# Kernel tuning notes

Hardware: AMD Instinct MI355X
Metric: run time of the kernel (lower is better)

Reference implementation:

```python
import jax, jax.numpy as jnp
import numpy as np

L = 4000      # num identities
C = 8         # num cameras; center bank is label-major: center j -> (label j//C, cam j%C)
T = 0.07      # temperature
HARD_NEG_K = 50
LAMDA = 0.5


def setup_inputs() -> dict:
    key = jax.random.key(0)
    k1, k2, k3, k4 = jax.random.split(key, 4)
    n, d = 256, 2048
    feats = jax.random.normal(k1, (n, d), dtype=jnp.float32)
    centers = jax.random.normal(k2, (L * C, d), dtype=jnp.float32)
    centers = centers / jnp.linalg.norm(centers, axis=1, keepdims=True)  # bank is kept unit-norm
    labels = jax.random.randint(k3, (n,), 0, L, dtype=jnp.int64)
    camids = jax.random.randint(k4, (n,), 0, C, dtype=jnp.int64)
    return {"feats": feats, "centers": centers, "labels": labels, "camids": camids, "epoch": 5}


def _cap_losses(feats, centers, labels, camids):
    n = feats.shape[0]
    M = centers.shape[0]
    feats = feats / jnp.linalg.norm(feats, axis=1, keepdims=True)  # F.normalize(p=2, dim=1)
    center_labels = jnp.arange(M) // C
    center_cams = jnp.arange(M) % C

    sims = jnp.einsum('nd,md->nm', feats, centers) / T  # [n, M] scaled similarities
    own_idx = labels * C + camids                        # cam_label_index[(label, cam)]
    own = sims[jnp.arange(n), own_idx]                   # numerator logits
    exp_sims = jnp.exp(sims)                             # unit vectors => sims <= 1/T ~ 14.3, safe

    # ---- intra-camera loss: denominator over centers sharing the sample's camid ----
    cam_mask = (center_cams[None, :] == camids[:, None])
    denom_intra = jnp.sum(exp_sims * cam_mask, axis=1)
    loss_i = own - jnp.log(denom_intra)                  # log(frac_up/frac_down)
    # mean per camid, then sum over camids present in the batch, negated
    ones = jnp.ones((n,), dtype=feats.dtype)
    cam_sums = jax.ops.segment_sum(loss_i, camids, num_segments=C)
    cam_cnts = jax.ops.segment_sum(ones, camids, num_segments=C)
    loss_intra = -jnp.sum(jnp.where(cam_cnts > 0, cam_sums / jnp.maximum(cam_cnts, 1.0), 0.0))

    # ---- inter loss: same-label centers + first-K hard negatives (in bank order) ----
    lbl_mask = (center_labels[None, :] == labels[:, None])
    other = ~lbl_mask
    # torch concatenates other-label centers in label order and takes the FIRST 50 (a slice,
    # not top-k); label-major bank order makes that = first 50 other-label centers by index.
    rank = jnp.cumsum(other.astype(jnp.int32), axis=1)
    hard_mask = other & (rank <= HARD_NEG_K)
    denom_inter = jnp.sum(exp_sims * lbl_mask, axis=1) + jnp.sum(exp_sims * hard_mask, axis=1)
    loss_j = own - jnp.log(denom_inter)
    lbl_sums = jax.ops.segment_sum(loss_j, labels, num_segments=L)
    lbl_cnts = jax.ops.segment_sum(ones, labels, num_segments=L)
    loss_inter = -jnp.sum(jnp.where(lbl_cnts > 0, lbl_sums / jnp.maximum(lbl_cnts, 1.0), 0.0))

    return loss_intra, loss_inter


def reference(feats, centers, labels, camids, epoch):
    loss_intra, loss_inter = _cap_losses(feats, centers, labels, camids)
    if epoch < 5:  # epoch is a static python int
        return loss_intra
    return jnp.stack([loss_intra, LAMDA * loss_inter])
```

## Files before the change

kernel.cpp:

```cpp
#include <hip/hip_runtime.h>

typedef __attribute__((ext_vector_type(8))) __bf16 bf16x8;
typedef __attribute__((ext_vector_type(4))) __bf16 bf16x4;
typedef __attribute__((ext_vector_type(4))) float f32x4;

#define N_SAMP 256
#define DIM    2048
#define NCENT  32000
#define INV_T  14.285714285714285714f
#define NWG    250

__global__ __launch_bounds__(256) void norm_kernel(const float* __restrict__ feats,
                                                   __bf16* __restrict__ fnorm,
                                                   float* __restrict__ d_acc) {
    int row = blockIdx.x;
    int tid = threadIdx.x;
    if (row < 16) d_acc[row * 256 + tid] = 0.f;
    const float* src = feats + (size_t)row * DIM;
    float4 v0 = reinterpret_cast<const float4*>(src)[2 * tid];
    float4 v1 = reinterpret_cast<const float4*>(src)[2 * tid + 1];
    float ss = v0.x * v0.x + v0.y * v0.y + v0.z * v0.z + v0.w * v0.w
             + v1.x * v1.x + v1.y * v1.y + v1.z * v1.z + v1.w * v1.w;
    #pragma unroll
    for (int off = 1; off < 64; off <<= 1) ss += __shfl_xor(ss, off, 64);
    __shared__ float wsum[4];
    if ((tid & 63) == 0) wsum[tid >> 6] = ss;
    __syncthreads();
    float inv = 1.0f / sqrtf(wsum[0] + wsum[1] + wsum[2] + wsum[3]);
    bf16x8 o;
    o[0] = (__bf16)(v0.x * inv); o[1] = (__bf16)(v0.y * inv);
    o[2] = (__bf16)(v0.z * inv); o[3] = (__bf16)(v0.w * inv);
    o[4] = (__bf16)(v1.x * inv); o[5] = (__bf16)(v1.y * inv);
    o[6] = (__bf16)(v1.z * inv); o[7] = (__bf16)(v1.w * inv);
    *reinterpret_cast<bf16x8*>(fnorm + (size_t)row * DIM + tid * 8) = o;
}

__global__ __launch_bounds__(512, 2) void sims_kernel(
    const __bf16* __restrict__ fnorm, const float* __restrict__ centers,
    const int* __restrict__ labels, const int* __restrict__ camids,
    float* __restrict__ d_acc, float* __restrict__ d_own)
{
    __shared__ __align__(16) char sA[2][16384];
    __shared__ __align__(16) char sB[2][8192];

    const int tid  = threadIdx.x;
    const int wave = tid >> 6;
    const int lane = tid & 63;
    const int l15  = lane & 15;
    const int lhi  = lane >> 4;

    const int nb    = blockIdx.x;
    const int cbase = nb * 128;

    const int wr = (wave >> 1) * 64;
    const int wc = (wave & 1) * 64;

    f32x4 acc[4][4] = {};

    const float4* bsrc = reinterpret_cast<const float4*>(centers);
    const uint4*  asrc = reinterpret_cast<const uint4*>(fnorm);

    auto issue = [&](int step, float4& b0, float4& b1, uint4& a0, uint4& a1) {
        int rb0 = tid >> 3, p = tid & 7;
        b0 = bsrc[(size_t)(cbase + rb0) * 512 + step * 8 + p];
        int rb1 = 64 + rb0;
        b1 = bsrc[(size_t)(cbase + rb1) * 512 + step * 8 + p];
        int ra0 = tid >> 2, pa = tid & 3;
        a0 = asrc[(size_t)ra0 * 256 + step * 4 + pa];
        int ra1 = 128 + ra0;
        a1 = asrc[(size_t)ra1 * 256 + step * 4 + pa];
    };
    auto wrbuf = [&](int b, const float4& b0, const float4& b1,
                     const uint4& a0, const uint4& a1) {
        #pragma unroll
        for (int j = 0; j < 2; ++j) {
            const float4& v = j ? b1 : b0;
            int row = j * 64 + (tid >> 3), pos = tid & 7;
            int adr = (row * 64 + pos * 8) ^ ((row & 7) << 4);
            bf16x4 o;
            o[0] = (__bf16)v.x; o[1] = (__bf16)v.y;
            o[2] = (__bf16)v.z; o[3] = (__bf16)v.w;
            *reinterpret_cast<uint2*>(&sB[b][adr]) = __builtin_bit_cast(uint2, o);
        }
        #pragma unroll
        for (int j = 0; j < 2; ++j) {
            const uint4& v = j ? a1 : a0;
            int row = j * 128 + (tid >> 2), pos = tid & 3;
            int adr = (row * 64 + pos * 16) ^ ((row & 7) << 4);
            *reinterpret_cast<uint4*>(&sA[b][adr]) = v;
        }
    };
    auto compute = [&](int b) {
        bf16x8 af[4], bf[4];
        #pragma unroll
        for (int mi = 0; mi < 4; ++mi) {
            int row = wr + mi * 16 + l15;
            int adr = (row * 64 + lhi * 16) ^ ((row & 7) << 4);
            af[mi] = *reinterpret_cast<const bf16x8*>(&sA[b][adr]);
        }
        #pragma unroll
        for (int ni = 0; ni < 4; ++ni) {
            int row = wc + ni * 16 + l15;
            int adr = (row * 64 + lhi * 16) ^ ((row & 7) << 4);
            bf[ni] = *reinterpret_cast<const bf16x8*>(&sB[b][adr]);
        }
        #pragma unroll
        for (int mi = 0; mi < 4; ++mi)
            #pragma unroll
            for (int ni = 0; ni < 4; ++ni)
                acc[mi][ni] = __builtin_amdgcn_mfma_f32_16x16x32_bf16(
                    af[mi], bf[ni], acc[mi][ni], 0, 0, 0);
    };
    #define BAR() do { asm volatile("s_waitcnt lgkmcnt(0)" ::: "memory"); \
                       __builtin_amdgcn_s_barrier(); } while (0)

    float4 b0A, b1A, b0B, b1B;
    uint4  a0A, a1A, a0B, a1B;

    issue(0, b0A, b1A, a0A, a1A);
    issue(1, b0B, b1B, a0B, a1B);
    wrbuf(0, b0A, b1A, a0A, a1A);
    BAR();
    for (int t = 0; t < 64; t += 2) {
        if (t + 2 < 64) issue(t + 2, b0A, b1A, a0A, a1A);
        compute(0);
        wrbuf(1, b0B, b1B, a0B, a1B);
        BAR();
        if (t + 3 < 64) issue(t + 3, b0B, b1B, a0B, a1B);
        compute(1);
        if (t + 2 < 64) {
            wrbuf(0, b0A, b1A, a0A, a1A);
            BAR();
        }
    }

    float* slot = d_acc + (nb & 7) * 512;
    #pragma unroll
    for (int mi = 0; mi < 4; ++mi) {
        #pragma unroll
        for (int r = 0; r < 4; ++r) {
            int i   = wr + mi * 16 + lhi * 4 + r;
            int lab = labels[i], cam = camids[i];
            int oidx = lab * 8 + cam;
            float pi = 0.f, pj = 0.f;
            #pragma unroll
            for (int ni = 0; ni < 4; ++ni) {
                int c = cbase + wc + ni * 16 + l15;
                float s = acc[mi][ni][r] * INV_T;
                float e = __expf(s);
                if ((l15 & 7) == cam) pi += e;
                bool ol = ((c >> 3) == lab);
                bool hard = (!ol) && (c < ((c < lab * 8) ? 50 : 58));
                if (ol || hard) pj += e;
                if (c == oidx) d_own[i] = s;
            }
            #pragma unroll
            for (int off = 1; off < 16; off <<= 1) {
                pi += __shfl_xor(pi, off, 64);
                pj += __shfl_xor(pj, off, 64);
            }
            if (l15 == 0) {
                atomicAdd(&slot[i], pi);
                atomicAdd(&slot[N_SAMP + i], pj);
            }
        }
    }
}

__global__ __launch_bounds__(256) void finalize_kernel(
    const float* __restrict__ d_acc, const float* __restrict__ d_own,
    const int* __restrict__ labels, const int* __restrict__ camids,
    float* __restrict__ out, int out_size)
{
    __shared__ int s_lab[N_SAMP], s_cam[N_SAMP];
    __shared__ float wsum[8];
    int tid = threadIdx.x;
    s_lab[tid] = labels[tid];
    s_cam[tid] = camids[tid];
    __syncthreads();
    int myl = s_lab[tid], myc = s_cam[tid];
    int nl = 0, nc = 0;
    for (int j = 0; j < N_SAMP; ++j) {
        nl += (s_lab[j] == myl);
        nc += (s_cam[j] == myc);
    }
    float di = 0.f, dj = 0.f;
    #pragma unroll
    for (int s = 0; s < 8; ++s) {
        di += d_acc[s * 512 + tid];
        dj += d_acc[s * 512 + 256 + tid];
    }
    float own = d_own[tid];
    float li = own - logf(di);
    float lj = own - logf(dj);
    float a = li / (float)nc;
    float b = lj / (float)nl;
    #pragma unroll
    for (int off = 1; off < 64; off <<= 1) {
        a += __shfl_xor(a, off, 64);
        b += __shfl_xor(b, off, 64);
    }
    if ((tid & 63) == 0) { wsum[tid >> 6] = a; wsum[4 + (tid >> 6)] = b; }
    __syncthreads();
    if (tid == 0) {
        float sa = wsum[0] + wsum[1] + wsum[2] + wsum[3];
        float sb = wsum[4] + wsum[5] + wsum[6] + wsum[7];
        out[0] = -sa;
        if (out_size > 1) out[1] = -0.5f * sb;
    }
}

extern "C" void kernel_launch(void* const* d_in, const int* in_sizes, int n_in,
                              void* d_out, int out_size, void* d_ws, size_t ws_size,
                              hipStream_t stream) {
    const float* feats   = (const float*)d_in[0];
    const float* centers = (const float*)d_in[1];
    const int*   labels  = (const int*)d_in[2];
    const int*   camids  = (const int*)d_in[3];
    float* out = (float*)d_out;

    __bf16* fnorm = (__bf16*)d_ws;
    float* d_acc  = (float*)((char*)d_ws + (size_t)N_SAMP * DIM * sizeof(__bf16));
    float* d_own  = d_acc + 8 * 2 * N_SAMP;

    norm_kernel<<<N_SAMP, 256, 0, stream>>>(feats, fnorm, d_acc);
    sims_kernel<<<NWG, 512, 0, stream>>>(fnorm, centers, labels, camids, d_acc, d_own);
    finalize_kernel<<<1, 256, 0, stream>>>(d_acc, d_own, labels, camids, out, out_size);
}
```

Measured before the change: 86.05 us.

## Pre-swizzle A tiles, load via global_load_lds, triple-buffer B, fuse finalize

The norm kernel now writes normalized features in a pre-swizzled tile layout, so the GEMM kernel can stream A directly into LDS with global_load_lds instead of staging through registers. B (centers) becomes triple-buffered with one 16-byte store per thread, and uses vmcnt-based waits, setprio around the MFMAs and a fully unrolled loop. The separate finalize launch is replaced by a last-block ticket reduction inside the sims kernel, which removes one kernel launch at the cost of an atomic ticket and threadfences. The fused tail reuses sB shared memory for the finalize scratch.

Measured after the change: 130.7 us. 1.52x slower.

```diff
diff --git a/kernel.cpp b/kernel.cpp
--- a/kernel.cpp
+++ b/kernel.cpp
@@ -1,7 +1,6 @@
 #include <hip/hip_runtime.h>
 
 typedef __attribute__((ext_vector_type(8))) __bf16 bf16x8;
-typedef __attribute__((ext_vector_type(4))) __bf16 bf16x4;
 typedef __attribute__((ext_vector_type(4))) float f32x4;
 
 #define N_SAMP 256
@@ -9,13 +8,17 @@
 #define NCENT  32000
 #define INV_T  14.285714285714285714f
 #define NWG    250
+#define NTILE  64
+
 
 __global__ __launch_bounds__(256) void norm_kernel(const float* __restrict__ feats,
-                                                   __bf16* __restrict__ fnorm,
-                                                   float* __restrict__ d_acc) {
+                                                   char* __restrict__ fnorm_sw,
+                                                   float* __restrict__ d_acc,
+                                                   int* __restrict__ ticket) {
     int row = blockIdx.x;
     int tid = threadIdx.x;
     if (row < 16) d_acc[row * 256 + tid] = 0.f;
+    if (row == 16 && tid == 0) *ticket = 0;
     const float* src = feats + (size_t)row * DIM;
     float4 v0 = reinterpret_cast<const float4*>(src)[2 * tid];
     float4 v1 = reinterpret_cast<const float4*>(src)[2 * tid + 1];
@@ -32,16 +35,20 @@
     o[2] = (__bf16)(v0.z * inv); o[3] = (__bf16)(v0.w * inv);
     o[4] = (__bf16)(v1.x * inv); o[5] = (__bf16)(v1.y * inv);
     o[6] = (__bf16)(v1.z * inv); o[7] = (__bf16)(v1.w * inv);
-    *reinterpret_cast<bf16x8*>(fnorm + (size_t)row * DIM + tid * 8) = o;
+    int tile = tid >> 2, c8 = tid & 3;
+    int pair = row >> 1;
+    int slot = (((row & 1) << 2) | c8) ^ (pair & 7);
+    *reinterpret_cast<bf16x8*>(fnorm_sw + (size_t)tile * 16384 + pair * 128 + slot * 16) = o;
 }
 
 __global__ __launch_bounds__(512, 2) void sims_kernel(
-    const __bf16* __restrict__ fnorm, const float* __restrict__ centers,
+    const char* __restrict__ fnorm_sw, const float* __restrict__ centers,
     const int* __restrict__ labels, const int* __restrict__ camids,
-    float* __restrict__ d_acc, float* __restrict__ d_own)
+    float* __restrict__ d_acc, float* __restrict__ d_own,
+    int* __restrict__ ticket, float* __restrict__ out, int out_size)
 {
     __shared__ __align__(16) char sA[2][16384];
-    __shared__ __align__(16) char sB[2][8192];
+    __shared__ __align__(16) char sB[3][8192];
 
     const int tid  = threadIdx.x;
     const int wave = tid >> 6;
@@ -58,83 +65,84 @@
     f32x4 acc[4][4] = {};
 
     const float4* bsrc = reinterpret_cast<const float4*>(centers);
-    const uint4*  asrc = reinterpret_cast<const uint4*>(fnorm);
-
-    auto issue = [&](int step, float4& b0, float4& b1, uint4& a0, uint4& a1) {
-        int rb0 = tid >> 3, p = tid & 7;
-        b0 = bsrc[(size_t)(cbase + rb0) * 512 + step * 8 + p];
-        int rb1 = 64 + rb0;
-        b1 = bsrc[(size_t)(cbase + rb1) * 512 + step * 8 + p];
-        int ra0 = tid >> 2, pa = tid & 3;
-        a0 = asrc[(size_t)ra0 * 256 + step * 4 + pa];
-        int ra1 = 128 + ra0;
-        a1 = asrc[(size_t)ra1 * 256 + step * 4 + pa];
-    };
-    auto wrbuf = [&](int b, const float4& b0, const float4& b1,
-                     const uint4& a0, const uint4& a1) {
-        #pragma unroll
-        for (int j = 0; j < 2; ++j) {
-            const float4& v = j ? b1 : b0;
-            int row = j * 64 + (tid >> 3), pos = tid & 7;
-            int adr = (row * 64 + pos * 8) ^ ((row & 7) << 4);
-            bf16x4 o;
-            o[0] = (__bf16)v.x; o[1] = (__bf16)v.y;
-            o[2] = (__bf16)v.z; o[3] = (__bf16)v.w;
-            *reinterpret_cast<uint2*>(&sB[b][adr]) = __builtin_bit_cast(uint2, o);
-        }
-        #pragma unroll
-        for (int j = 0; j < 2; ++j) {
-            const uint4& v = j ? a1 : a0;
-            int row = j * 128 + (tid >> 2), pos = tid & 3;
-            int adr = (row * 64 + pos * 16) ^ ((row & 7) << 4);
-            *reinterpret_cast<uint4*>(&sA[b][adr]) = v;
-        }
-    };
-    auto compute = [&](int b) {
+
+    const int bP = tid >> 3, bs = tid & 7;
+    const int bu = bs ^ (bP & 7);
+    const int brow = 2 * bP + (bu >> 2);
+    const int bc8  = bu & 3;
+    const size_t bbase = (size_t)(cbase + brow) * 512 + bc8 * 2;
+
+    auto issueB = [&](int T, float4& f0, float4& f1) {
+        f0 = bsrc[bbase + T * 8];
+        f1 = bsrc[bbase + T * 8 + 1];
+    };
+    auto wrbufB = [&](int buf, const float4& f0, const float4& f1) {
+        bf16x8 o;
+        o[0] = (__bf16)f0.x; o[1] = (__bf16)f0.y; o[2] = (__bf16)f0.z; o[3] = (__bf16)f0.w;
+        o[4] = (__bf16)f1.x; o[5] = (__bf16)f1.y; o[6] = (__bf16)f1.z; o[7] = (__bf16)f1.w;
+        *reinterpret_cast<bf16x8*>(&sB[buf][tid * 16]) = o;
+    };
+    auto aLds = [&](int T, int buf) {
+        const char* src = fnorm_sw + (size_t)T * 16384 + (wave * 2) * 1024 + lane * 16;
+        __builtin_amdgcn_global_load_lds((const unsigned int*)src,
+                                         (unsigned int*)&sA[buf][(wave * 2) * 1024], 16, 0, 0);
+        __builtin_amdgcn_global_load_lds((const unsigned int*)(src + 1024),
+                                         (unsigned int*)&sA[buf][(wave * 2 + 1) * 1024], 16, 0, 0);
+    };
+    auto compute = [&](int bufA, int bufB) {
         bf16x8 af[4], bf[4];
         #pragma unroll
         for (int mi = 0; mi < 4; ++mi) {
-            int row = wr + mi * 16 + l15;
-            int adr = (row * 64 + lhi * 16) ^ ((row & 7) << 4);
-            af[mi] = *reinterpret_cast<const bf16x8*>(&sA[b][adr]);
+            int row = wr + mi * 16 + l15, pair = row >> 1;
+            int slot = (((row & 1) << 2) | lhi) ^ (pair & 7);
+            af[mi] = *reinterpret_cast<const bf16x8*>(&sA[bufA][pair * 128 + slot * 16]);
         }
         #pragma unroll
         for (int ni = 0; ni < 4; ++ni) {
-            int row = wc + ni * 16 + l15;
-            int adr = (row * 64 + lhi * 16) ^ ((row & 7) << 4);
-            bf[ni] = *reinterpret_cast<const bf16x8*>(&sB[b][adr]);
-        }
+            int row = wc + ni * 16 + l15, pair = row >> 1;
+            int slot = (((row & 1) << 2) | lhi) ^ (pair & 7);
+            bf[ni] = *reinterpret_cast<const bf16x8*>(&sB[bufB][pair * 128 + slot * 16]);
+        }
+        __builtin_amdgcn_s_setprio(1);
         #pragma unroll
         for (int mi = 0; mi < 4; ++mi)
             #pragma unroll
             for (int ni = 0; ni < 4; ++ni)
                 acc[mi][ni] = __builtin_amdgcn_mfma_f32_16x16x32_bf16(
                     af[mi], bf[ni], acc[mi][ni], 0, 0, 0);
-    };
-    #define BAR() do { asm volatile("s_waitcnt lgkmcnt(0)" ::: "memory"); \
-                       __builtin_amdgcn_s_barrier(); } while (0)
-
-    float4 b0A, b1A, b0B, b1B;
-    uint4  a0A, a1A, a0B, a1B;
-
-    issue(0, b0A, b1A, a0A, a1A);
-    issue(1, b0B, b1B, a0B, a1B);
-    wrbuf(0, b0A, b1A, a0A, a1A);
-    BAR();
-    for (int t = 0; t < 64; t += 2) {
-        if (t + 2 < 64) issue(t + 2, b0A, b1A, a0A, a1A);
-        compute(0);
-        wrbuf(1, b0B, b1B, a0B, a1B);
-        BAR();
-        if (t + 3 < 64) issue(t + 3, b0B, b1B, a0B, a1B);
-        compute(1);
-        if (t + 2 < 64) {
-            wrbuf(0, b0A, b1A, a0A, a1A);
-            BAR();
+        __builtin_amdgcn_s_setprio(0);
+    };
+
+    float4 b0S0, b1S0, b0S1, b1S1;
+
+    issueB(0, b0S0, b1S0);
+    issueB(1, b0S1, b1S1);
+    aLds(0, 0);
+    wrbufB(0, b0S0, b1S0);
+    asm volatile("s_waitcnt vmcnt(0)" ::: "memory");
+    asm volatile("s_waitcnt lgkmcnt(0)" ::: "memory");
+    __builtin_amdgcn_s_barrier();
+
+    #pragma unroll
+    for (int t = 0; t < NTILE; ++t) {
+        const int cur = t & 1;
+        if (t + 1 < NTILE) aLds(t + 1, cur ^ 1);
+        if (t + 2 < NTILE) {
+            if (((t + 2) & 1) == 0) issueB(t + 2, b0S0, b1S0);
+            else                    issueB(t + 2, b0S1, b1S1);
+        }
+        compute(cur, t % 3);
+        if (t + 1 < NTILE) {
+            if (((t + 1) & 1) == 0) wrbufB((t + 1) % 3, b0S0, b1S0);
+            else                    wrbufB((t + 1) % 3, b0S1, b1S1);
+            if (t + 2 < NTILE) asm volatile("s_waitcnt vmcnt(2)" ::: "memory");
+            else               asm volatile("s_waitcnt vmcnt(0)" ::: "memory");
+            asm volatile("s_waitcnt lgkmcnt(0)" ::: "memory");
+            __builtin_amdgcn_s_barrier();
         }
     }
 
-    float* slot = d_acc + (nb & 7) * 512;
+    float* slot_acc = d_acc + (nb & 7) * 512;
     #pragma unroll
     for (int mi = 0; mi < 4; ++mi) {
         #pragma unroll
@@ -160,53 +168,57 @@
                 pj += __shfl_xor(pj, off, 64);
             }
             if (l15 == 0) {
-                atomicAdd(&slot[i], pi);
-                atomicAdd(&slot[N_SAMP + i], pj);
+                atomicAdd(&slot_acc[i], pi);
+                atomicAdd(&slot_acc[N_SAMP + i], pj);
             }
         }
     }
-}
-
-__global__ __launch_bounds__(256) void finalize_kernel(
-    const float* __restrict__ d_acc, const float* __restrict__ d_own,
-    const int* __restrict__ labels, const int* __restrict__ camids,
-    float* __restrict__ out, int out_size)
-{
-    __shared__ int s_lab[N_SAMP], s_cam[N_SAMP];
-    __shared__ float wsum[8];
-    int tid = threadIdx.x;
-    s_lab[tid] = labels[tid];
-    s_cam[tid] = camids[tid];
+
+    __threadfence();
     __syncthreads();
-    int myl = s_lab[tid], myc = s_cam[tid];
-    int nl = 0, nc = 0;
-    for (int j = 0; j < N_SAMP; ++j) {
-        nl += (s_lab[j] == myl);
-        nc += (s_cam[j] == myc);
-    }
-    float di = 0.f, dj = 0.f;
-    #pragma unroll
-    for (int s = 0; s < 8; ++s) {
-        di += d_acc[s * 512 + tid];
-        dj += d_acc[s * 512 + 256 + tid];
-    }
-    float own = d_own[tid];
-    float li = own - logf(di);
-    float lj = own - logf(dj);
-    float a = li / (float)nc;
-    float b = lj / (float)nl;
-    #pragma unroll
-    for (int off = 1; off < 64; off <<= 1) {
-        a += __shfl_xor(a, off, 64);
-        b += __shfl_xor(b, off, 64);
-    }
-    if ((tid & 63) == 0) { wsum[tid >> 6] = a; wsum[4 + (tid >> 6)] = b; }
+    __shared__ int s_last;
+    if (tid == 0) s_last = (atomicAdd(ticket, 1) == NWG - 1) ? 1 : 0;
     __syncthreads();
-    if (tid == 0) {
-        float sa = wsum[0] + wsum[1] + wsum[2] + wsum[3];
-        float sb = wsum[4] + wsum[5] + wsum[6] + wsum[7];
-        out[0] = -sa;
-        if (out_size > 1) out[1] = -0.5f * sb;
+    if (s_last) {
+        __threadfence();
+        int* s_lab = (int*)&sB[0][0];
+        int* s_cam = s_lab + 256;
+        float* wsum = (float*)(s_cam + 256);
+        if (tid < 256) { s_lab[tid] = labels[tid]; s_cam[tid] = camids[tid]; }
+        __syncthreads();
+        float a = 0.f, b = 0.f;
+        if (tid < 256) {
+            int myl = s_lab[tid], myc = s_cam[tid];
+            int nl = 0, nc = 0;
+            for (int j = 0; j < 256; ++j) {
+                nl += (s_lab[j] == myl);
+                nc += (s_cam[j] == myc);
+            }
+            float di = 0.f, dj = 0.f;
+            #pragma unroll
+            for (int s = 0; s < 8; ++s) {
+                di += d_acc[s * 512 + tid];
+                dj += d_acc[s * 512 + 256 + tid];
+            }
+            float own = d_own[tid];
+            a = (own - logf(di)) / (float)nc;
+            b = (own - logf(dj)) / (float)nl;
+        }
+        #pragma unroll
+        for (int off = 1; off < 64; off <<= 1) {
+            a += __shfl_xor(a, off, 64);
+            b += __shfl_xor(b, off, 64);
+        }
+        if ((tid & 63) == 0) { wsum[tid >> 6] = a; wsum[8 + (tid >> 6)] = b; }
+        __syncthreads();
+        if (tid == 0) {
+            float sa = wsum[0] + wsum[1] + wsum[2] + wsum[3]
+                     + wsum[4] + wsum[5] + wsum[6] + wsum[7];
+            float sb = wsum[8] + wsum[9] + wsum[10] + wsum[11]
+                     + wsum[12] + wsum[13] + wsum[14] + wsum[15];
+            out[0] = -sa;
+            if (out_size > 1) out[1] = -0.5f * sb;
+        }
     }
 }
 
@@ -219,11 +231,12 @@
     const int*   camids  = (const int*)d_in[3];
     float* out = (float*)d_out;
 
-    __bf16* fnorm = (__bf16*)d_ws;
-    float* d_acc  = (float*)((char*)d_ws + (size_t)N_SAMP * DIM * sizeof(__bf16));
-    float* d_own  = d_acc + 8 * 2 * N_SAMP;
-
-    norm_kernel<<<N_SAMP, 256, 0, stream>>>(feats, fnorm, d_acc);
-    sims_kernel<<<NWG, 512, 0, stream>>>(fnorm, centers, labels, camids, d_acc, d_own);
-    finalize_kernel<<<1, 256, 0, stream>>>(d_acc, d_own, labels, camids, out, out_size);
+    char*  fnorm_sw = (char*)d_ws;
+    float* d_acc    = (float*)((char*)d_ws + (size_t)1048576);
+    float* d_own    = d_acc + 8 * 2 * N_SAMP;
+    int*   ticket   = (int*)(d_own + N_SAMP);
+
+    norm_kernel<<<N_SAMP, 256, 0, stream>>>(feats, fnorm_sw, d_acc, ticket);
+    sims_kernel<<<NWG, 512, 0, stream>>>(fnorm_sw, centers, labels, camids,
+                                         d_acc, d_own, ticket, out, out_size);
 }
```

## Pre-pack normalized features in MFMA fragment order and load A directly to registers

Applied to the files above, without the earlier changes.

The norm kernel now writes the bf16 normalized features in a layout that matches the MFMA A-fragment order, so each wave loads its A operands straight from global memory (L2-resident) into registers without staging through LDS. The sA shared buffer goes away, which frees LDS and removes A writes and reads around each barrier. The B loads are rearranged so each thread loads two contiguous float4 and writes one 16-byte bf16x8 with an XOR swizzle. The trade-off is that global A loads now sit on the compute path and depend on L2 latency being hidden by the double-buffered register prefetch.

Measured after the change: 89.55 us. +4.1%, slower.

```diff
diff --git a/kernel.cpp b/kernel.cpp
--- a/kernel.cpp
+++ b/kernel.cpp
@@ -1,7 +1,6 @@
 #include <hip/hip_runtime.h>
 
 typedef __attribute__((ext_vector_type(8))) __bf16 bf16x8;
-typedef __attribute__((ext_vector_type(4))) __bf16 bf16x4;
 typedef __attribute__((ext_vector_type(4))) float f32x4;
 
 #define N_SAMP 256
@@ -9,9 +8,11 @@
 #define NCENT  32000
 #define INV_T  14.285714285714285714f
 #define NWG    250
+#define NTILE  64
+
 
 __global__ __launch_bounds__(256) void norm_kernel(const float* __restrict__ feats,
-                                                   __bf16* __restrict__ fnorm,
+                                                   char* __restrict__ fnorm_pk,
                                                    float* __restrict__ d_acc) {
     int row = blockIdx.x;
     int tid = threadIdx.x;
@@ -32,15 +33,18 @@
     o[2] = (__bf16)(v0.z * inv); o[3] = (__bf16)(v0.w * inv);
     o[4] = (__bf16)(v1.x * inv); o[5] = (__bf16)(v1.y * inv);
     o[6] = (__bf16)(v1.z * inv); o[7] = (__bf16)(v1.w * inv);
-    *reinterpret_cast<bf16x8*>(fnorm + (size_t)row * DIM + tid * 8) = o;
+    int tile = tid >> 2, ksub = tid & 3;
+    int grp  = row >> 4;
+    int lane = (row & 15) | (ksub << 4);
+    *reinterpret_cast<bf16x8*>(fnorm_pk
+        + ((size_t)tile * 16 + grp) * 1024 + lane * 16) = o;
 }
 
 __global__ __launch_bounds__(512, 2) void sims_kernel(
-    const __bf16* __restrict__ fnorm, const float* __restrict__ centers,
+    const char* __restrict__ fnorm_pk, const float* __restrict__ centers,
     const int* __restrict__ labels, const int* __restrict__ camids,
     float* __restrict__ d_acc, float* __restrict__ d_own)
 {
-    __shared__ __align__(16) char sA[2][16384];
     __shared__ __align__(16) char sB[2][8192];
 
     const int tid  = threadIdx.x;
@@ -58,51 +62,38 @@
     f32x4 acc[4][4] = {};
 
     const float4* bsrc = reinterpret_cast<const float4*>(centers);
-    const uint4*  asrc = reinterpret_cast<const uint4*>(fnorm);
-
-    auto issue = [&](int step, float4& b0, float4& b1, uint4& a0, uint4& a1) {
-        int rb0 = tid >> 3, p = tid & 7;
-        b0 = bsrc[(size_t)(cbase + rb0) * 512 + step * 8 + p];
-        int rb1 = 64 + rb0;
-        b1 = bsrc[(size_t)(cbase + rb1) * 512 + step * 8 + p];
-        int ra0 = tid >> 2, pa = tid & 3;
-        a0 = asrc[(size_t)ra0 * 256 + step * 4 + pa];
-        int ra1 = 128 + ra0;
-        a1 = asrc[(size_t)ra1 * 256 + step * 4 + pa];
-    };
-    auto wrbuf = [&](int b, const float4& b0, const float4& b1,
-                     const uint4& a0, const uint4& a1) {
-        #pragma unroll
-        for (int j = 0; j < 2; ++j) {
-            const float4& v = j ? b1 : b0;
-            int row = j * 64 + (tid >> 3), pos = tid & 7;
-            int adr = (row * 64 + pos * 8) ^ ((row & 7) << 4);
-            bf16x4 o;
-            o[0] = (__bf16)v.x; o[1] = (__bf16)v.y;
-            o[2] = (__bf16)v.z; o[3] = (__bf16)v.w;
-            *reinterpret_cast<uint2*>(&sB[b][adr]) = __builtin_bit_cast(uint2, o);
-        }
-        #pragma unroll
-        for (int j = 0; j < 2; ++j) {
-            const uint4& v = j ? a1 : a0;
-            int row = j * 128 + (tid >> 2), pos = tid & 3;
-            int adr = (row * 64 + pos * 16) ^ ((row & 7) << 4);
-            *reinterpret_cast<uint4*>(&sA[b][adr]) = v;
-        }
-    };
-    auto compute = [&](int b) {
-        bf16x8 af[4], bf[4];
-        #pragma unroll
-        for (int mi = 0; mi < 4; ++mi) {
-            int row = wr + mi * 16 + l15;
-            int adr = (row * 64 + lhi * 16) ^ ((row & 7) << 4);
-            af[mi] = *reinterpret_cast<const bf16x8*>(&sA[b][adr]);
-        }
+    const char*   apk  = fnorm_pk + ((size_t)(wave >> 1) * 4) * 1024 + lane * 16;
+
+    const int bP = tid >> 3, bs = tid & 7;
+    const int bu = bs ^ (bP & 7);
+    const int brow = 2 * bP + (bu >> 2);
+    const int bc8  = bu & 3;
+    const size_t bbase = (size_t)(cbase + brow) * 512 + bc8 * 2;
+
+    auto issueB = [&](int T, float4& f0, float4& f1) {
+        f0 = bsrc[bbase + T * 8];
+        f1 = bsrc[bbase + T * 8 + 1];
+    };
+    auto wrbufB = [&](int buf, const float4& f0, const float4& f1) {
+        bf16x8 o;
+        o[0] = (__bf16)f0.x; o[1] = (__bf16)f0.y; o[2] = (__bf16)f0.z; o[3] = (__bf16)f0.w;
+        o[4] = (__bf16)f1.x; o[5] = (__bf16)f1.y; o[6] = (__bf16)f1.z; o[7] = (__bf16)f1.w;
+        *reinterpret_cast<bf16x8*>(&sB[buf][tid * 16]) = o;
+    };
+    auto issueA = [&](int T, bf16x8 (&af)[4]) {
+        const char* p = apk + (size_t)T * 16384;
+        af[0] = *reinterpret_cast<const bf16x8*>(p);
+        af[1] = *reinterpret_cast<const bf16x8*>(p + 1024);
+        af[2] = *reinterpret_cast<const bf16x8*>(p + 2048);
+        af[3] = *reinterpret_cast<const bf16x8*>(p + 3072);
+    };
+    auto compute = [&](int buf, const bf16x8 (&af)[4]) {
+        bf16x8 bf[4];
         #pragma unroll
         for (int ni = 0; ni < 4; ++ni) {
-            int row = wc + ni * 16 + l15;
-            int adr = (row * 64 + lhi * 16) ^ ((row & 7) << 4);
-            bf[ni] = *reinterpret_cast<const bf16x8*>(&sB[b][adr]);
+            int row = wc + ni * 16 + l15, pair = row >> 1;
+            int slot = (((row & 1) << 2) | lhi) ^ (pair & 7);
+            bf[ni] = *reinterpret_cast<const bf16x8*>(&sB[buf][pair * 128 + slot * 16]);
         }
         #pragma unroll
         for (int mi = 0; mi < 4; ++mi)
@@ -114,27 +105,30 @@
     #define BAR() do { asm volatile("s_waitcnt lgkmcnt(0)" ::: "memory"); \
                        __builtin_amdgcn_s_barrier(); } while (0)
 
-    float4 b0A, b1A, b0B, b1B;
-    uint4  a0A, a1A, a0B, a1B;
-
-    issue(0, b0A, b1A, a0A, a1A);
-    issue(1, b0B, b1B, a0B, a1B);
-    wrbuf(0, b0A, b1A, a0A, a1A);
+    float4 b0S0, b1S0, b0S1, b1S1;
+    bf16x8 afA[4], afB[4];
+
+    issueB(0, b0S0, b1S0);
+    issueB(1, b0S1, b1S1);
+    issueA(0, afA);
+    wrbufB(0, b0S0, b1S0);
     BAR();
-    for (int t = 0; t < 64; t += 2) {
-        if (t + 2 < 64) issue(t + 2, b0A, b1A, a0A, a1A);
-        compute(0);
-        wrbuf(1, b0B, b1B, a0B, a1B);
+    for (int t = 0; t < NTILE; t += 2) {
+        if (t + 2 < NTILE) issueB(t + 2, b0S0, b1S0);
+        issueA(t + 1, afB);
+        compute(0, afA);
+        wrbufB(1, b0S1, b1S1);
         BAR();
-        if (t + 3 < 64) issue(t + 3, b0B, b1B, a0B, a1B);
-        compute(1);
-        if (t + 2 < 64) {
-            wrbuf(0, b0A, b1A, a0A, a1A);
+        if (t + 3 < NTILE) issueB(t + 3, b0S1, b1S1);
+        if (t + 2 < NTILE) issueA(t + 2, afA);
+        compute(1, afB);
+        if (t + 2 < NTILE) {
+            wrbufB(0, b0S0, b1S0);
             BAR();
         }
     }
 
-    float* slot = d_acc + (nb & 7) * 512;
+    float* slot_acc = d_acc + (nb & 7) * 512;
     #pragma unroll
     for (int mi = 0; mi < 4; ++mi) {
         #pragma unroll
@@ -160,8 +154,8 @@
                 pj += __shfl_xor(pj, off, 64);
             }
             if (l15 == 0) {
-                atomicAdd(&slot[i], pi);
-                atomicAdd(&slot[N_SAMP + i], pj);
+                atomicAdd(&slot_acc[i], pi);
+                atomicAdd(&slot_acc[N_SAMP + i], pj);
             }
         }
     }
@@ -219,11 +213,11 @@
     const int*   camids  = (const int*)d_in[3];
     float* out = (float*)d_out;
 
-    __bf16* fnorm = (__bf16*)d_ws;
-    float* d_acc  = (float*)((char*)d_ws + (size_t)N_SAMP * DIM * sizeof(__bf16));
-    float* d_own  = d_acc + 8 * 2 * N_SAMP;
-
-    norm_kernel<<<N_SAMP, 256, 0, stream>>>(feats, fnorm, d_acc);
-    sims_kernel<<<NWG, 512, 0, stream>>>(fnorm, centers, labels, camids, d_acc, d_own);
+    char*  fnorm_pk = (char*)d_ws;
+    float* d_acc    = (float*)((char*)d_ws + (size_t)1048576);
+    float* d_own    = d_acc + 8 * 2 * N_SAMP;
+
+    norm_kernel<<<N_SAMP, 256, 0, stream>>>(feats, fnorm_pk, d_acc);
+    sims_kernel<<<NWG, 512, 0, stream>>>(fnorm_pk, centers, labels, camids, d_acc, d_own);
     finalize_kernel<<<1, 256, 0, stream>>>(d_acc, d_own, labels, camids, out, out_size);
 }
```
